# Optimization experiments

Measured on AMD Instinct MI355X. Metric: run time of the kernel, lower is better.

Reference implementation:

```python
import jax, jax.numpy as jnp
import numpy as np

B, L, D, H, E = 2, 2048, 1024, 4096, 8
CAP = int(1.25 * 2 * (B * L) / E)  # top-2 capacity = 1280


def setup_inputs() -> dict:
    key = jax.random.key(0)
    k0, k1, k2, k3 = jax.random.split(key, 4)
    gate_std = (0.1 / D) ** 0.5
    return {
        "inputs": jax.random.normal(k0, (B, L, D), jnp.float32),
        "gate_weight": jax.random.normal(k1, (E, D), jnp.float32) * gate_std,
        "w1": jax.random.normal(k2, (E, D, H), jnp.float32) * 0.02,
        "b1": jnp.zeros((E, 1, H), jnp.float32),
        "w2": jax.random.normal(k3, (E, H, D), jnp.float32) * 0.02,
        "b2": jnp.zeros((E, 1, D), jnp.float32),
    }


def reference(inputs, gate_weight, w1, b1, w2, b2):
    tokens = inputs.reshape(-1, D)                      # [S, D], S = B*L
    # gate computed in fp32 as in original
    logits = tokens.astype(jnp.float32) @ gate_weight.astype(jnp.float32).T  # [S, E]
    gates = jax.nn.softmax(logits, axis=-1)

    # top-2 routing
    top1 = jnp.argmax(gates, axis=-1)
    mask1 = jax.nn.one_hot(top1, E, dtype=jnp.float32)  # [S, E]
    gates_wo1 = jnp.where(mask1 > 0, -jnp.inf, gates)
    top2 = jnp.argmax(gates_wo1, axis=-1)
    mask2 = jax.nn.one_hot(top2, E, dtype=jnp.float32)

    # load-balancing aux loss (GShard style, pre-capacity masks)
    me = jnp.mean(gates, axis=0)
    ce = jnp.mean(mask1, axis=0)
    l_aux = E * jnp.sum(me * ce)

    # capacity positions via cumulative sum per expert
    loc1 = jnp.cumsum(mask1, axis=0) - 1.0              # [S, E]
    loc2 = jnp.cumsum(mask2, axis=0) - 1.0 + jnp.sum(mask1, axis=0, keepdims=True)
    mask1 = mask1 * (loc1 < CAP)
    mask2 = mask2 * (loc2 < CAP)

    gate1 = jnp.sum(gates * mask1, axis=-1)             # [S]
    gate2 = jnp.sum(gates * mask2, axis=-1)
    denom = jnp.maximum(gate1 + gate2, jnp.finfo(jnp.float32).eps)
    wgt1 = gate1 / denom
    wgt2 = gate2 / denom

    pos1 = jnp.sum(loc1 * mask1, axis=-1).astype(jnp.int32)  # [S]
    pos2 = jnp.sum(loc2 * mask2, axis=-1).astype(jnp.int32)
    cap1 = jax.nn.one_hot(pos1, CAP, dtype=jnp.float32)      # [S, C]
    cap2 = jax.nn.one_hot(pos2, CAP, dtype=jnp.float32)

    # combine weights [S, E, C] and dispatch mask
    combine = (wgt1[:, None, None] * mask1[:, :, None] * cap1[:, None, :]
               + wgt2[:, None, None] * mask2[:, :, None] * cap2[:, None, :])
    sec_mask_f = (combine > 0).astype(inputs.dtype)

    # dispatch: [E, C, S] @ [S, D] -> [E, C, D]
    dispatch = jnp.einsum('sec,sd->ecd', sec_mask_f, tokens)

    # per-expert FFN (batched over experts)
    h = jax.nn.gelu(jnp.einsum('ecd,edh->ech', dispatch, w1) + b1)
    expert_out = jnp.einsum('ech,ehd->ecd', h, w2) + b2

    # combine: [S, E*C] @ [E*C, D] -> [S, D]
    ans = jnp.einsum('sec,ecd->sd', combine.astype(inputs.dtype), expert_out)
    return ans.reshape(inputs.shape), l_aux
```

## Files before the change

### kernel.cpp

```cpp
#include <hip/hip_runtime.h>

#define S_TOK 4096
#define DMODEL 1024
#define HDIM 4096
#define NEXP 8
#define CAPACITY 1280

struct TokenRoute { int e1, p1, e2, p2; float w1, w2; };

typedef __bf16 bf16x8 __attribute__((ext_vector_type(8)));
typedef float f32x4 __attribute__((ext_vector_type(4)));
typedef unsigned short ushort8v __attribute__((ext_vector_type(8)));

__device__ __forceinline__ unsigned short f2bf(float f) {
    unsigned int u = __float_as_uint(f);
    unsigned int r = 0x7fffu + ((u >> 16) & 1u);
    return (unsigned short)((u + r) >> 16);
}
__device__ __forceinline__ float bf2f(unsigned short b) {
    return __uint_as_float(((unsigned int)b) << 16);
}

__device__ __forceinline__ void gload16(const void* gsrc, void* ldst) {
    __builtin_amdgcn_global_load_lds(
        (const __attribute__((address_space(1))) unsigned int*)gsrc,
        (__attribute__((address_space(3))) unsigned int*)ldst, 16, 0, 0);
}

template <int N> __device__ __forceinline__ void wait_vmcnt() {
    if constexpr (N == 0) asm volatile("s_waitcnt vmcnt(0)" ::: "memory");
    else if constexpr (N == 6) asm volatile("s_waitcnt vmcnt(6)" ::: "memory");
    else if constexpr (N == 8) asm volatile("s_waitcnt vmcnt(8)" ::: "memory");
}

__device__ __forceinline__ float gelu_f(float x) {
    float u = x * (0.7978845608028654f + 0.0356774081363f * x * x);
    return x / (1.0f + __expf(-2.0f * u));
}

__global__ void transpose_cvt(const float* __restrict__ src, unsigned short* __restrict__ dst,
                              int R, int C) {
    __shared__ unsigned short t[64][66];
    size_t eoff = (size_t)blockIdx.z * R * C;
    int r0 = blockIdx.y * 64, c0 = blockIdx.x * 64, tid = threadIdx.x;
    int rr = tid >> 4, cq = (tid & 15) * 4;
#pragma unroll
    for (int p = 0; p < 4; ++p) {
        int row = p * 16 + rr;
        float4 v = *(const float4*)(src + eoff + (size_t)(r0 + row) * C + c0 + cq);
        t[row][cq + 0] = f2bf(v.x); t[row][cq + 1] = f2bf(v.y);
        t[row][cq + 2] = f2bf(v.z); t[row][cq + 3] = f2bf(v.w);
    }
    __syncthreads();
    int k0 = (tid & 7) * 8;
#pragma unroll
    for (int pp = 0; pp < 2; ++pp) {
        int oc = pp * 32 + (tid >> 3);
        ushort8v o;
#pragma unroll
        for (int x = 0; x < 8; ++x) o[x] = t[k0 + x][oc];
        *(ushort8v*)(dst + eoff + (size_t)(c0 + oc) * R + r0 + k0) = o;
    }
}

__global__ void gate_kernel(const float* __restrict__ tokens, const float* __restrict__ gw,
                            float* __restrict__ gates, TokenRoute* __restrict__ route) {
    int s = blockIdx.x, l = threadIdx.x;
    const float* x = tokens + (size_t)s * DMODEL;
    float p[NEXP];
#pragma unroll
    for (int e = 0; e < NEXP; ++e) p[e] = 0.f;
#pragma unroll
    for (int it = 0; it < 4; ++it) {
        int i = (it * 64 + l) * 4;
        float4 v = *(const float4*)(x + i);
#pragma unroll
        for (int e = 0; e < NEXP; ++e) {
            float4 g = *(const float4*)(gw + e * DMODEL + i);
            p[e] += v.x * g.x + v.y * g.y + v.z * g.z + v.w * g.w;
        }
    }
#pragma unroll
    for (int e = 0; e < NEXP; ++e) {
        float v = p[e];
        v += __shfl_xor(v, 32); v += __shfl_xor(v, 16); v += __shfl_xor(v, 8);
        v += __shfl_xor(v, 4);  v += __shfl_xor(v, 2);  v += __shfl_xor(v, 1);
        p[e] = v;
    }
    int e1 = 0; float b1v = p[0];
#pragma unroll
    for (int e = 1; e < NEXP; ++e) if (p[e] > b1v) { b1v = p[e]; e1 = e; }
    int e2 = -1; float b2v = -3.0e38f;
#pragma unroll
    for (int e = 0; e < NEXP; ++e) if (e != e1 && p[e] > b2v) { b2v = p[e]; e2 = e; }
    float mx = p[0];
#pragma unroll
    for (int e = 1; e < NEXP; ++e) mx = fmaxf(mx, p[e]);
    float sum = 0.f;
#pragma unroll
    for (int e = 0; e < NEXP; ++e) { p[e] = __expf(p[e] - mx); sum += p[e]; }
    float inv = 1.0f / sum;
#pragma unroll
    for (int e = 0; e < NEXP; ++e) p[e] *= inv;
    float g1 = __expf(b1v - mx) * inv;
    float g2 = __expf(b2v - mx) * inv;
    if (l == 0) {
        float* gp = gates + (size_t)s * NEXP;
#pragma unroll
        for (int e = 0; e < NEXP; ++e) gp[e] = p[e];
        TokenRoute r; r.e1 = e1; r.p1 = 0; r.e2 = e2; r.p2 = 0; r.w1 = g1; r.w2 = g2;
        route[s] = r;
    }
}

__device__ __forceinline__ unsigned ext16(unsigned long long lo, unsigned long long hi, int e) {
    unsigned long long q = (e < 4) ? lo : hi;
    return (unsigned)((q >> ((e & 3) * 16)) & 0xFFFFULL);
}

__global__ __launch_bounds__(1024)
void route_scan(TokenRoute* __restrict__ route, const float* __restrict__ gates,
                int* __restrict__ cnt, float* __restrict__ laux_out) {
    __shared__ unsigned long long wt[16][4];
    __shared__ float fsum[16][NEXP];
    int t = threadIdx.x, wid = t >> 6, ln = t & 63;
    TokenRoute tr[4];
    unsigned long long own[4] = {0, 0, 0, 0};
#pragma unroll
    for (int j = 0; j < 4; ++j) {
        tr[j] = route[t * 4 + j];
        int e1 = tr[j].e1, e2 = tr[j].e2;
        if (e1 < 4) own[0] += 1ULL << (e1 * 16); else own[1] += 1ULL << ((e1 - 4) * 16);
        if (e2 < 4) own[2] += 1ULL << (e2 * 16); else own[3] += 1ULL << ((e2 - 4) * 16);
    }
    unsigned long long inc[4] = {own[0], own[1], own[2], own[3]};
#pragma unroll
    for (int off = 1; off < 64; off <<= 1) {
#pragma unroll
        for (int q = 0; q < 4; ++q) {
            unsigned long long v = __shfl_up(inc[q], off);
            if (ln >= off) inc[q] += v;
        }
    }
    if (ln == 63) {
#pragma unroll
        for (int q = 0; q < 4; ++q) wt[wid][q] = inc[q];
    }
    __syncthreads();
    unsigned long long woff[4] = {0, 0, 0, 0}, tot[4] = {0, 0, 0, 0};
    for (int w = 0; w < 16; ++w) {
#pragma unroll
        for (int q = 0; q < 4; ++q) {
            unsigned long long v = wt[w][q];
            tot[q] += v;
            if (w < wid) woff[q] += v;
        }
    }
    unsigned long long ex[4];
#pragma unroll
    for (int q = 0; q < 4; ++q) ex[q] = woff[q] + inc[q] - own[q];

    float gs[NEXP];
#pragma unroll
    for (int e = 0; e < NEXP; ++e) gs[e] = 0.f;
#pragma unroll
    for (int j = 0; j < 4; ++j) {
        const float* gp = gates + (size_t)(t * 4 + j) * NEXP;
#pragma unroll
        for (int e = 0; e < NEXP; ++e) gs[e] += gp[e];
    }
#pragma unroll
    for (int e = 0; e < NEXP; ++e) {
        float v = gs[e];
        v += __shfl_xor(v, 32); v += __shfl_xor(v, 16); v += __shfl_xor(v, 8);
        v += __shfl_xor(v, 4);  v += __shfl_xor(v, 2);  v += __shfl_xor(v, 1);
        gs[e] = v;
    }
    if (ln == 0) {
#pragma unroll
        for (int e = 0; e < NEXP; ++e) fsum[wid][e] = gs[e];
    }
    __syncthreads();
    if (t == 0) {
        float laux = 0.f;
#pragma unroll
        for (int e = 0; e < NEXP; ++e) {
            float m = 0.f;
            for (int w = 0; w < 16; ++w) m += fsum[w][e];
            unsigned t1 = ext16(tot[0], tot[1], e);
            unsigned t2 = ext16(tot[2], tot[3], e);
            laux += (m / (float)S_TOK) * ((float)t1 / (float)S_TOK);
            int c = (int)(t1 + t2);
            cnt[e] = c < CAPACITY ? c : CAPACITY;
        }
        *laux_out = laux * (float)NEXP;
    }
    unsigned long long r1lo = ex[0], r1hi = ex[1], r2lo = ex[2], r2hi = ex[3];
#pragma unroll
    for (int j = 0; j < 4; ++j) {
        int e1 = tr[j].e1, e2 = tr[j].e2;
        unsigned loc1 = ext16(r1lo, r1hi, e1);
        if (e1 < 4) r1lo += 1ULL << (e1 * 16); else r1hi += 1ULL << ((e1 - 4) * 16);
        unsigned loc2 = ext16(r2lo, r2hi, e2) + ext16(tot[0], tot[1], e2);
        if (e2 < 4) r2lo += 1ULL << (e2 * 16); else r2hi += 1ULL << ((e2 - 4) * 16);
        bool k1 = loc1 < CAPACITY, k2 = loc2 < CAPACITY;
        float G1 = k1 ? tr[j].w1 : 0.f;
        float G2 = k2 ? tr[j].w2 : 0.f;
        float denom = fmaxf(G1 + G2, 1.1920929e-07f);
        TokenRoute r;
        r.e1 = e1; r.p1 = k1 ? (int)loc1 : -1;
        r.e2 = e2; r.p2 = k2 ? (int)loc2 : -1;
        r.w1 = G1 / denom; r.w2 = G2 / denom;
        route[t * 4 + j] = r;
    }
}

__global__ void dispatch_scatter(const float* __restrict__ tokens, const TokenRoute* __restrict__ route,
                                 unsigned short* __restrict__ disp) {
    int s = blockIdx.x, l = threadIdx.x;
    TokenRoute r = route[s];
    const float* x = tokens + (size_t)s * DMODEL;
    ushort4 vals[4];
#pragma unroll
    for (int q = 0; q < 4; ++q) {
        float4 v = *(const float4*)(x + (q * 64 + l) * 4);
        vals[q].x = f2bf(v.x); vals[q].y = f2bf(v.y); vals[q].z = f2bf(v.z); vals[q].w = f2bf(v.w);
    }
    if (r.p1 >= 0) {
        unsigned short* d = disp + ((size_t)r.e1 * CAPACITY + r.p1) * DMODEL;
#pragma unroll
        for (int q = 0; q < 4; ++q) *(ushort4*)(d + (q * 64 + l) * 4) = vals[q];
    }
    if (r.p2 >= 0) {
        unsigned short* d = disp + ((size_t)r.e2 * CAPACITY + r.p2) * DMODEL;
#pragma unroll
        for (int q = 0; q < 4; ++q) *(ushort4*)(d + (q * 64 + l) * 4) = vals[q];
    }
}

template <int BN, int WM, int WN, int MODE>
__global__ __launch_bounds__(512, 2)
void gemm256(const unsigned short* __restrict__ A, const unsigned short* __restrict__ Bt,
             unsigned short* __restrict__ C, const float* __restrict__ bias,
             const int* __restrict__ cnt,
             int N, int K, int Ntiles,
             size_t strideAe, size_t strideBe, size_t strideCe, int biasStride) {
    constexpr int MF = 256 / WM / 16;
    constexpr int NF = BN / WN / 16;
    constexpr int RW = 256 / WM;
    constexpr int CW = BN / WN;
    constexpr int NBJ = BN / 64;
    constexpr int LPT = 4 + NBJ;
    constexpr int ASLOT = 256 * 64;
    constexpr int BSLOT = BN * 64;

    __shared__ unsigned short slds[(2 * 256 + 2 * BN) * 64];

    int e = blockIdx.z;
    int mt = blockIdx.x / Ntiles, nt = blockIdx.x % Ntiles;
    if (mt * 256 >= cnt[e]) return;
    const unsigned short* Ae = A + (size_t)e * strideAe;
    const unsigned short* Be = Bt + (size_t)e * strideBe;
    unsigned short* Ce = C + (size_t)e * strideCe;
    const float* be = bias + (size_t)e * biasStride;

    int tid = threadIdx.x;
    int wv = tid >> 6, ln = tid & 63;
    int wm = wv / WN, wn = wv % WN;
    int lr = ln & 15, kc = ln >> 4;
    int rsw = lr & 7;

    size_t gOffA[4]; int ldsA[4];
#pragma unroll
    for (int j = 0; j < 4; ++j) {
        int g = (wv * 4 + j) * 64 + ln;
        int row = g >> 3, cl = g & 7, cs = cl ^ (row & 7);
        ldsA[j] = (wv * 4 + j) * 512;
        gOffA[j] = (size_t)(mt * 256 + row) * K + cs * 8;
    }
    size_t gOffB[NBJ]; int ldsB[NBJ];
#pragma unroll
    for (int j = 0; j < NBJ; ++j) {
        int g = (wv * NBJ + j) * 64 + ln;
        int row = g >> 3, cl = g & 7, cs = cl ^ (row & 7);
        ldsB[j] = (wv * NBJ + j) * 512;
        gOffB[j] = (size_t)(nt * BN + row) * K + cs * 8;
    }
    int aoff[MF], boff[NF];
#pragma unroll
    for (int i = 0; i < MF; ++i) aoff[i] = (wm * RW + i * 16 + lr) * 64;
#pragma unroll
    for (int j = 0; j < NF; ++j) boff[j] = (wn * CW + j * 16 + lr) * 64;
    int chk0 = ((kc) ^ rsw) * 8;
    int chk1 = ((kc + 4) ^ rsw) * 8;

    f32x4 acc[MF][NF];
#pragma unroll
    for (int i = 0; i < MF; ++i)
#pragma unroll
        for (int j = 0; j < NF; ++j) acc[i][j] = (f32x4){0.f, 0.f, 0.f, 0.f};

    auto stage = [&](int slot, int kt) {
        unsigned short* da = slds + slot * ASLOT;
        unsigned short* db = slds + 2 * ASLOT + slot * BSLOT;
#pragma unroll
        for (int j = 0; j < 4; ++j) gload16(Ae + gOffA[j] + kt * 64, da + ldsA[j]);
#pragma unroll
        for (int j = 0; j < NBJ; ++j) gload16(Be + gOffB[j] + kt * 64, db + ldsB[j]);
    };

    int nk = K >> 6;
    stage(0, 0);
    stage(1, 1);
    wait_vmcnt<LPT>();
    __builtin_amdgcn_s_barrier();

    int cur = 0;
    for (int kt = 0; kt < nk; ++kt) {
        const unsigned short* sa = slds + cur * ASLOT;
        const unsigned short* sb = slds + 2 * ASLOT + cur * BSLOT;
        __builtin_amdgcn_s_setprio(1);
#pragma unroll
        for (int s = 0; s < 2; ++s) {
            int ck = (s == 0) ? chk0 : chk1;
            bf16x8 av[MF], bv[NF];
#pragma unroll
            for (int i = 0; i < MF; ++i) av[i] = *(const bf16x8*)(sa + aoff[i] + ck);
#pragma unroll
            for (int j = 0; j < NF; ++j) bv[j] = *(const bf16x8*)(sb + boff[j] + ck);
#pragma unroll
            for (int i = 0; i < MF; ++i)
#pragma unroll
                for (int j = 0; j < NF; ++j)
                    acc[i][j] = __builtin_amdgcn_mfma_f32_16x16x32_bf16(av[i], bv[j], acc[i][j], 0, 0, 0);
        }
        __builtin_amdgcn_s_setprio(0);
        __builtin_amdgcn_sched_barrier(0);
        __builtin_amdgcn_s_barrier();
        if (kt + 2 < nk) stage(cur, kt + 2);
        if (kt + 1 < nk) {
            if (kt + 2 < nk) wait_vmcnt<LPT>(); else wait_vmcnt<0>();
            __builtin_amdgcn_s_barrier();
        }
        cur ^= 1;
    }

    __syncthreads();
    unsigned short* scratch = slds + wv * (RW * CW);
    float bvj[NF];
#pragma unroll
    for (int j = 0; j < NF; ++j) bvj[j] = be[nt * BN + wn * CW + j * 16 + lr];
#pragma unroll
    for (int i = 0; i < MF; ++i) {
#pragma unroll
        for (int j = 0; j < NF; ++j) {
            int col_l = j * 16 + lr;
#pragma unroll
            for (int r = 0; r < 4; ++r) {
                int row_l = i * 16 + kc * 4 + r;
                float v = acc[i][j][r] + bvj[j];
                if (MODE == 0) v = gelu_f(v);
                scratch[row_l * CW + col_l] = f2bf(v);
            }
        }
    }
    int rrow = ln >> 3, rcol = (ln & 7) * 8;
#pragma unroll
    for (int p = 0; p < RW / 8; ++p) {
        int row_l = p * 8 + rrow;
        ushort8v v = *(const ushort8v*)&scratch[row_l * CW + rcol];
        int row_g = mt * 256 + wm * RW + row_l;
        int col_g = nt * BN + wn * CW + rcol;
        *(ushort8v*)&Ce[(size_t)row_g * N + col_g] = v;
    }
}

__global__ void combine_kernel(const TokenRoute* __restrict__ route, const unsigned short* __restrict__ eout,
                               float* __restrict__ out) {
    int s = blockIdx.x, l = threadIdx.x;
    TokenRoute r = route[s];
    bool v1 = r.p1 >= 0, v2 = r.p2 >= 0;
#pragma unroll
    for (int q = 0; q < 4; ++q) {
        int i = (q * 64 + l) * 4;
        float4 a = {0.f, 0.f, 0.f, 0.f};
        if (v1) {
            const unsigned short* p = eout + ((size_t)r.e1 * CAPACITY + r.p1) * DMODEL + i;
            ushort4 u = *(const ushort4*)p;
            a.x += r.w1 * bf2f(u.x); a.y += r.w1 * bf2f(u.y);
            a.z += r.w1 * bf2f(u.z); a.w += r.w1 * bf2f(u.w);
        }
        if (v2) {
            const unsigned short* p = eout + ((size_t)r.e2 * CAPACITY + r.p2) * DMODEL + i;
            ushort4 u = *(const ushort4*)p;
            a.x += r.w2 * bf2f(u.x); a.y += r.w2 * bf2f(u.y);
            a.z += r.w2 * bf2f(u.z); a.w += r.w2 * bf2f(u.w);
        }
        *(float4*)(out + (size_t)s * DMODEL + i) = a;
    }
}

extern "C" void kernel_launch(void* const* d_in, const int* in_sizes, int n_in,
                              void* d_out, int out_size, void* d_ws, size_t ws_size,
                              hipStream_t stream) {
    const float* inputs = (const float*)d_in[0];
    const float* gw     = (const float*)d_in[1];
    const float* w1     = (const float*)d_in[2];
    const float* b1     = (const float*)d_in[3];
    const float* w2     = (const float*)d_in[4];
    const float* b2     = (const float*)d_in[5];
    float* out = (float*)d_out;

    char* ws = (char*)d_ws;
    const size_t SZ_W = (size_t)NEXP * DMODEL * HDIM * 2;
    const size_t SZ_DISP = (size_t)NEXP * CAPACITY * DMODEL * 2;
    const size_t SZ_H = (size_t)NEXP * CAPACITY * HDIM * 2;
    unsigned short* wb1t = (unsigned short*)(ws);
    unsigned short* wb2t = (unsigned short*)(ws + SZ_W);
    unsigned short* disp = (unsigned short*)(ws + 2 * SZ_W);
    unsigned short* h    = (unsigned short*)(ws + 2 * SZ_W + SZ_DISP);
    float* gates = (float*)(ws + 2 * SZ_W + SZ_DISP + SZ_H);
    TokenRoute* route = (TokenRoute*)(ws + 2 * SZ_W + SZ_DISP + SZ_H + (size_t)S_TOK * NEXP * 4);
    int* cnt = (int*)((char*)route + (size_t)S_TOK * sizeof(TokenRoute));

    transpose_cvt<<<dim3(HDIM / 64, DMODEL / 64, NEXP), 256, 0, stream>>>(w1, wb1t, DMODEL, HDIM);
    transpose_cvt<<<dim3(DMODEL / 64, HDIM / 64, NEXP), 256, 0, stream>>>(w2, wb2t, HDIM, DMODEL);
    gate_kernel<<<S_TOK, 64, 0, stream>>>(inputs, gw, gates, route);
    route_scan<<<1, 1024, 0, stream>>>(route, gates, cnt, out + (size_t)S_TOK * DMODEL);
    dispatch_scatter<<<S_TOK, 64, 0, stream>>>(inputs, route, disp);
    gemm256<256, 2, 4, 0><<<dim3((CAPACITY / 256 + 1) * (HDIM / 256), 1, NEXP), 512, 0, stream>>>(
        disp, wb1t, h, b1, cnt, HDIM, DMODEL, HDIM / 256,
        (size_t)CAPACITY * DMODEL, (size_t)HDIM * DMODEL, (size_t)CAPACITY * HDIM, HDIM);
    gemm256<128, 4, 2, 1><<<dim3((CAPACITY / 256 + 1) * (DMODEL / 128), 1, NEXP), 512, 0, stream>>>(
        h, wb2t, disp, b2, cnt, DMODEL, HDIM, DMODEL / 128,
        (size_t)CAPACITY * HDIM, (size_t)DMODEL * HDIM, (size_t)CAPACITY * DMODEL, DMODEL);
    combine_kernel<<<S_TOK, 64, 0, stream>>>(route, disp, out);
}
```

Baseline: 642.5 us.

## Replace dispatch scatter with gathered GEMM, new triple-buffered 256x128 GEMM, fused gate+bf16 cvt

Removes the dispatch_scatter kernel. Tokens are converted to bf16 inside the gate kernel, and the first expert GEMM gathers rows through an index table built by a new idx_fill kernel. Both GEMMs move to a new 256-thread kernel with a 256x128 tile, K-step 32, a three-slot LDS pipeline, a row-pair swizzled layout and an XCD-aware block remap. The weight transpose kernel is rewritten for wider LDS accesses, and the expert output reuses the w1 workspace. Risks: gathered loads are less coalesced, and padded capacity rows index tokens through masked garbage indices.

After: 582.2 us. 9.4% less time.

```diff
diff --git a/kernel.cpp b/kernel.cpp
--- a/kernel.cpp
+++ b/kernel.cpp
@@ -30,7 +30,6 @@
 template <int N> __device__ __forceinline__ void wait_vmcnt() {
     if constexpr (N == 0) asm volatile("s_waitcnt vmcnt(0)" ::: "memory");
     else if constexpr (N == 6) asm volatile("s_waitcnt vmcnt(6)" ::: "memory");
-    else if constexpr (N == 8) asm volatile("s_waitcnt vmcnt(8)" ::: "memory");
 }
 
 __device__ __forceinline__ float gelu_f(float x) {
@@ -38,34 +37,41 @@
     return x / (1.0f + __expf(-2.0f * u));
 }
 
-__global__ void transpose_cvt(const float* __restrict__ src, unsigned short* __restrict__ dst,
-                              int R, int C) {
-    __shared__ unsigned short t[64][66];
+__global__ __launch_bounds__(256) void transpose_cvt(const float* __restrict__ src,
+                                                     unsigned short* __restrict__ dst,
+                                                     int R, int C) {
+    __shared__ unsigned short t2[64][72];
     size_t eoff = (size_t)blockIdx.z * R * C;
     int r0 = blockIdx.y * 64, c0 = blockIdx.x * 64, tid = threadIdx.x;
-    int rr = tid >> 4, cq = (tid & 15) * 4;
-#pragma unroll
-    for (int p = 0; p < 4; ++p) {
-        int row = p * 16 + rr;
-        float4 v = *(const float4*)(src + eoff + (size_t)(r0 + row) * C + c0 + cq);
-        t[row][cq + 0] = f2bf(v.x); t[row][cq + 1] = f2bf(v.y);
-        t[row][cq + 2] = f2bf(v.z); t[row][cq + 3] = f2bf(v.w);
+    int q = tid & 15, g = tid >> 4;
+    float vr[4][4];
+#pragma unroll
+    for (int rr = 0; rr < 4; ++rr) {
+        float4 v = *(const float4*)(src + eoff + (size_t)(r0 + g * 4 + rr) * C + c0 + q * 4);
+        vr[rr][0] = v.x; vr[rr][1] = v.y; vr[rr][2] = v.z; vr[rr][3] = v.w;
+    }
+#pragma unroll
+    for (int cc = 0; cc < 4; ++cc) {
+        ushort4 o;
+        o.x = f2bf(vr[0][cc]); o.y = f2bf(vr[1][cc]);
+        o.z = f2bf(vr[2][cc]); o.w = f2bf(vr[3][cc]);
+        *(ushort4*)&t2[q * 4 + cc][g * 4] = o;
     }
     __syncthreads();
-    int k0 = (tid & 7) * 8;
-#pragma unroll
-    for (int pp = 0; pp < 2; ++pp) {
-        int oc = pp * 32 + (tid >> 3);
-        ushort8v o;
-#pragma unroll
-        for (int x = 0; x < 8; ++x) o[x] = t[k0 + x][oc];
-        *(ushort8v*)(dst + eoff + (size_t)(c0 + oc) * R + r0 + k0) = o;
-    }
-}
-
-__global__ void gate_kernel(const float* __restrict__ tokens, const float* __restrict__ gw,
-                            float* __restrict__ gates, TokenRoute* __restrict__ route) {
-    int s = blockIdx.x, l = threadIdx.x;
+    int orr = tid >> 2, seg = tid & 3;
+    ushort8v a = *(const ushort8v*)&t2[orr][seg * 16];
+    ushort8v b = *(const ushort8v*)&t2[orr][seg * 16 + 8];
+    unsigned short* dp = dst + eoff + (size_t)(c0 + orr) * R + r0 + seg * 16;
+    *(ushort8v*)dp = a;
+    *(ushort8v*)(dp + 8) = b;
+}
+
+__global__ __launch_bounds__(256)
+void gate_cvt(const float* __restrict__ tokens, const float* __restrict__ gw,
+              unsigned short* __restrict__ tok, float* __restrict__ gates,
+              TokenRoute* __restrict__ route) {
+    int wv = threadIdx.x >> 6, l = threadIdx.x & 63;
+    int s = blockIdx.x * 4 + wv;
     const float* x = tokens + (size_t)s * DMODEL;
     float p[NEXP];
 #pragma unroll
@@ -74,10 +80,12 @@
     for (int it = 0; it < 4; ++it) {
         int i = (it * 64 + l) * 4;
         float4 v = *(const float4*)(x + i);
+        ushort4 o; o.x = f2bf(v.x); o.y = f2bf(v.y); o.z = f2bf(v.z); o.w = f2bf(v.w);
+        *(ushort4*)(tok + (size_t)s * DMODEL + i) = o;
 #pragma unroll
         for (int e = 0; e < NEXP; ++e) {
-            float4 g = *(const float4*)(gw + e * DMODEL + i);
-            p[e] += v.x * g.x + v.y * g.y + v.z * g.z + v.w * g.w;
+            float4 gg = *(const float4*)(gw + e * DMODEL + i);
+            p[e] += v.x * gg.x + v.y * gg.y + v.z * gg.z + v.w * gg.w;
         }
     }
 #pragma unroll
@@ -215,162 +223,141 @@
     }
 }
 
-__global__ void dispatch_scatter(const float* __restrict__ tokens, const TokenRoute* __restrict__ route,
-                                 unsigned short* __restrict__ disp) {
-    int s = blockIdx.x, l = threadIdx.x;
+__global__ void idx_fill(const TokenRoute* __restrict__ route, int* __restrict__ idx) {
+    int s = blockIdx.x * 256 + threadIdx.x;
     TokenRoute r = route[s];
-    const float* x = tokens + (size_t)s * DMODEL;
-    ushort4 vals[4];
-#pragma unroll
-    for (int q = 0; q < 4; ++q) {
-        float4 v = *(const float4*)(x + (q * 64 + l) * 4);
-        vals[q].x = f2bf(v.x); vals[q].y = f2bf(v.y); vals[q].z = f2bf(v.z); vals[q].w = f2bf(v.w);
-    }
-    if (r.p1 >= 0) {
-        unsigned short* d = disp + ((size_t)r.e1 * CAPACITY + r.p1) * DMODEL;
-#pragma unroll
-        for (int q = 0; q < 4; ++q) *(ushort4*)(d + (q * 64 + l) * 4) = vals[q];
-    }
-    if (r.p2 >= 0) {
-        unsigned short* d = disp + ((size_t)r.e2 * CAPACITY + r.p2) * DMODEL;
-#pragma unroll
-        for (int q = 0; q < 4; ++q) *(ushort4*)(d + (q * 64 + l) * 4) = vals[q];
-    }
-}
-
-template <int BN, int WM, int WN, int MODE>
-__global__ __launch_bounds__(512, 2)
-void gemm256(const unsigned short* __restrict__ A, const unsigned short* __restrict__ Bt,
-             unsigned short* __restrict__ C, const float* __restrict__ bias,
-             const int* __restrict__ cnt,
-             int N, int K, int Ntiles,
-             size_t strideAe, size_t strideBe, size_t strideCe, int biasStride) {
-    constexpr int MF = 256 / WM / 16;
-    constexpr int NF = BN / WN / 16;
-    constexpr int RW = 256 / WM;
-    constexpr int CW = BN / WN;
-    constexpr int NBJ = BN / 64;
-    constexpr int LPT = 4 + NBJ;
-    constexpr int ASLOT = 256 * 64;
-    constexpr int BSLOT = BN * 64;
-
-    __shared__ unsigned short slds[(2 * 256 + 2 * BN) * 64];
-
-    int e = blockIdx.z;
-    int mt = blockIdx.x / Ntiles, nt = blockIdx.x % Ntiles;
+    if (r.p1 >= 0) idx[r.e1 * CAPACITY + r.p1] = s;
+    if (r.p2 >= 0) idx[r.e2 * CAPACITY + r.p2] = s;
+}
+
+template <int KEL, int NT, bool GATHER, int MODE>
+__global__ __launch_bounds__(256, 2)
+void gemm_ff(const unsigned short* __restrict__ A, const int* __restrict__ idx,
+             const unsigned short* __restrict__ B, unsigned short* __restrict__ C,
+             const float* __restrict__ bias, const int* __restrict__ cnt,
+             int N, size_t strideAe, size_t strideBe, size_t strideCe, int biasStride) {
+    constexpr int NK = KEL / 32;
+    __shared__ unsigned short slds[3 * 8192 + 3 * 4096];
+
+    constexpr int TOTAL = NEXP * 5 * NT;
+    int bid = blockIdx.x;
+    int nb = (bid & 7) * (TOTAL >> 3) + (bid >> 3);
+    int nt = nb % NT; int mt = (nb / NT) % 5; int e = nb / (NT * 5);
     if (mt * 256 >= cnt[e]) return;
-    const unsigned short* Ae = A + (size_t)e * strideAe;
-    const unsigned short* Be = Bt + (size_t)e * strideBe;
+
+    const unsigned short* Ae = GATHER ? A : (A + (size_t)e * strideAe);
+    const unsigned short* Be = B + (size_t)e * strideBe + (size_t)nt * 128 * KEL;
     unsigned short* Ce = C + (size_t)e * strideCe;
     const float* be = bias + (size_t)e * biasStride;
 
-    int tid = threadIdx.x;
-    int wv = tid >> 6, ln = tid & 63;
-    int wm = wv / WN, wn = wv % WN;
-    int lr = ln & 15, kc = ln >> 4;
-    int rsw = lr & 7;
-
-    size_t gOffA[4]; int ldsA[4];
+    int tid = threadIdx.x, wv = tid >> 6, ln = tid & 63;
+    int wm = wv >> 1, wn = wv & 1;
+    int lr = ln & 15, kc4 = ln >> 4;
+
+    const unsigned short* gAp[4]; int ldsA[4];
+#pragma unroll
+    for (int jj = 0; jj < 4; ++jj) {
+        int p = (wv * 4 + jj) * 64 + ln;
+        int lq = p >> 3, c = p & 7, u = c ^ (lq & 7);
+        int r = 2 * lq + (u >> 2), kcs = u & 3;
+        ldsA[jj] = p * 8;
+        if constexpr (GATHER) {
+            int tokr = idx[e * CAPACITY + mt * 256 + r] & (S_TOK - 1);
+            gAp[jj] = Ae + (size_t)tokr * KEL + kcs * 8;
+        } else {
+            gAp[jj] = Ae + (size_t)(mt * 256 + r) * KEL + kcs * 8;
+        }
+    }
+    const unsigned short* gBp[2]; int ldsB[2];
+#pragma unroll
+    for (int jj = 0; jj < 2; ++jj) {
+        int p = (wv * 2 + jj) * 64 + ln;
+        int lq = p >> 3, c = p & 7, u = c ^ (lq & 7);
+        int r = 2 * lq + (u >> 2), kcs = u & 3;
+        ldsB[jj] = p * 8;
+        gBp[jj] = Be + (size_t)r * KEL + kcs * 8;
+    }
+    int aoff[8], boff[4];
+#pragma unroll
+    for (int i = 0; i < 8; ++i) {
+        int row = wm * 128 + i * 16 + lr;
+        int lq = row >> 1, c = (((lr & 1) << 2) | kc4) ^ (lq & 7);
+        aoff[i] = lq * 64 + c * 8;
+    }
 #pragma unroll
     for (int j = 0; j < 4; ++j) {
-        int g = (wv * 4 + j) * 64 + ln;
-        int row = g >> 3, cl = g & 7, cs = cl ^ (row & 7);
-        ldsA[j] = (wv * 4 + j) * 512;
-        gOffA[j] = (size_t)(mt * 256 + row) * K + cs * 8;
-    }
-    size_t gOffB[NBJ]; int ldsB[NBJ];
-#pragma unroll
-    for (int j = 0; j < NBJ; ++j) {
-        int g = (wv * NBJ + j) * 64 + ln;
-        int row = g >> 3, cl = g & 7, cs = cl ^ (row & 7);
-        ldsB[j] = (wv * NBJ + j) * 512;
-        gOffB[j] = (size_t)(nt * BN + row) * K + cs * 8;
-    }
-    int aoff[MF], boff[NF];
-#pragma unroll
-    for (int i = 0; i < MF; ++i) aoff[i] = (wm * RW + i * 16 + lr) * 64;
-#pragma unroll
-    for (int j = 0; j < NF; ++j) boff[j] = (wn * CW + j * 16 + lr) * 64;
-    int chk0 = ((kc) ^ rsw) * 8;
-    int chk1 = ((kc + 4) ^ rsw) * 8;
-
-    f32x4 acc[MF][NF];
-#pragma unroll
-    for (int i = 0; i < MF; ++i)
-#pragma unroll
-        for (int j = 0; j < NF; ++j) acc[i][j] = (f32x4){0.f, 0.f, 0.f, 0.f};
-
-    auto stage = [&](int slot, int kt) {
-        unsigned short* da = slds + slot * ASLOT;
-        unsigned short* db = slds + 2 * ASLOT + slot * BSLOT;
-#pragma unroll
-        for (int j = 0; j < 4; ++j) gload16(Ae + gOffA[j] + kt * 64, da + ldsA[j]);
-#pragma unroll
-        for (int j = 0; j < NBJ; ++j) gload16(Be + gOffB[j] + kt * 64, db + ldsB[j]);
+        int row = wn * 64 + j * 16 + lr;
+        int lq = row >> 1, c = (((lr & 1) << 2) | kc4) ^ (lq & 7);
+        boff[j] = lq * 64 + c * 8;
+    }
+
+    f32x4 acc[8][4];
+#pragma unroll
+    for (int i = 0; i < 8; ++i)
+#pragma unroll
+        for (int j = 0; j < 4; ++j) acc[i][j] = (f32x4){0.f, 0.f, 0.f, 0.f};
+
+    auto stage = [&](int kt, int slot) {
+#pragma unroll
+        for (int jj = 0; jj < 4; ++jj)
+            gload16(gAp[jj] + kt * 32, &slds[slot * 8192 + ldsA[jj]]);
+#pragma unroll
+        for (int jj = 0; jj < 2; ++jj)
+            gload16(gBp[jj] + kt * 32, &slds[24576 + slot * 4096 + ldsB[jj]]);
     };
 
-    int nk = K >> 6;
     stage(0, 0);
     stage(1, 1);
-    wait_vmcnt<LPT>();
+    wait_vmcnt<6>();
     __builtin_amdgcn_s_barrier();
 
-    int cur = 0;
-    for (int kt = 0; kt < nk; ++kt) {
-        const unsigned short* sa = slds + cur * ASLOT;
-        const unsigned short* sb = slds + 2 * ASLOT + cur * BSLOT;
+    int sc = 0;
+    for (int kt = 0; kt < NK; ++kt) {
+        int s2 = sc + 2; if (s2 >= 3) s2 -= 3;
+        if (kt + 2 < NK) stage(kt + 2, s2);
+        bf16x8 av[8], bv[4];
+#pragma unroll
+        for (int i = 0; i < 8; ++i) av[i] = *(const bf16x8*)&slds[sc * 8192 + aoff[i]];
+#pragma unroll
+        for (int j = 0; j < 4; ++j) bv[j] = *(const bf16x8*)&slds[24576 + sc * 4096 + boff[j]];
         __builtin_amdgcn_s_setprio(1);
 #pragma unroll
-        for (int s = 0; s < 2; ++s) {
-            int ck = (s == 0) ? chk0 : chk1;
-            bf16x8 av[MF], bv[NF];
-#pragma unroll
-            for (int i = 0; i < MF; ++i) av[i] = *(const bf16x8*)(sa + aoff[i] + ck);
-#pragma unroll
-            for (int j = 0; j < NF; ++j) bv[j] = *(const bf16x8*)(sb + boff[j] + ck);
-#pragma unroll
-            for (int i = 0; i < MF; ++i)
-#pragma unroll
-                for (int j = 0; j < NF; ++j)
-                    acc[i][j] = __builtin_amdgcn_mfma_f32_16x16x32_bf16(av[i], bv[j], acc[i][j], 0, 0, 0);
-        }
+        for (int i = 0; i < 8; ++i)
+#pragma unroll
+            for (int j = 0; j < 4; ++j)
+                acc[i][j] = __builtin_amdgcn_mfma_f32_16x16x32_bf16(av[i], bv[j], acc[i][j], 0, 0, 0);
         __builtin_amdgcn_s_setprio(0);
-        __builtin_amdgcn_sched_barrier(0);
+        if (kt + 2 < NK) wait_vmcnt<6>();
+        else wait_vmcnt<0>();
         __builtin_amdgcn_s_barrier();
-        if (kt + 2 < nk) stage(cur, kt + 2);
-        if (kt + 1 < nk) {
-            if (kt + 2 < nk) wait_vmcnt<LPT>(); else wait_vmcnt<0>();
-            __builtin_amdgcn_s_barrier();
-        }
-        cur ^= 1;
+        sc = (sc == 2) ? 0 : sc + 1;
     }
 
     __syncthreads();
-    unsigned short* scratch = slds + wv * (RW * CW);
-    float bvj[NF];
-#pragma unroll
-    for (int j = 0; j < NF; ++j) bvj[j] = be[nt * BN + wn * CW + j * 16 + lr];
-#pragma unroll
-    for (int i = 0; i < MF; ++i) {
-#pragma unroll
-        for (int j = 0; j < NF; ++j) {
-            int col_l = j * 16 + lr;
+    unsigned short* scratch = slds + wv * 8192;
+    float bvj[4];
+#pragma unroll
+    for (int j = 0; j < 4; ++j) bvj[j] = be[nt * 128 + wn * 64 + j * 16 + lr];
+#pragma unroll
+    for (int i = 0; i < 8; ++i) {
+#pragma unroll
+        for (int j = 0; j < 4; ++j) {
 #pragma unroll
             for (int r = 0; r < 4; ++r) {
-                int row_l = i * 16 + kc * 4 + r;
-                float v = acc[i][j][r] + bvj[j];
-                if (MODE == 0) v = gelu_f(v);
-                scratch[row_l * CW + col_l] = f2bf(v);
+                float vv = acc[i][j][r] + bvj[j];
+                if (MODE == 0) vv = gelu_f(vv);
+                scratch[(i * 16 + kc4 * 4 + r) * 64 + j * 16 + lr] = f2bf(vv);
             }
         }
     }
+    __syncthreads();
     int rrow = ln >> 3, rcol = (ln & 7) * 8;
 #pragma unroll
-    for (int p = 0; p < RW / 8; ++p) {
+    for (int p = 0; p < 16; ++p) {
         int row_l = p * 8 + rrow;
-        ushort8v v = *(const ushort8v*)&scratch[row_l * CW + rcol];
-        int row_g = mt * 256 + wm * RW + row_l;
-        int col_g = nt * BN + wn * CW + rcol;
+        ushort8v v = *(const ushort8v*)&scratch[row_l * 64 + rcol];
+        int row_g = mt * 256 + wm * 128 + row_l;
+        int col_g = nt * 128 + wn * 64 + rcol;
         *(ushort8v*)&Ce[(size_t)row_g * N + col_g] = v;
     }
 }
@@ -412,27 +399,29 @@
     float* out = (float*)d_out;
 
     char* ws = (char*)d_ws;
-    const size_t SZ_W = (size_t)NEXP * DMODEL * HDIM * 2;
-    const size_t SZ_DISP = (size_t)NEXP * CAPACITY * DMODEL * 2;
-    const size_t SZ_H = (size_t)NEXP * CAPACITY * HDIM * 2;
+    const size_t SZ_W   = (size_t)NEXP * DMODEL * HDIM * 2;
+    const size_t SZ_H   = (size_t)NEXP * CAPACITY * HDIM * 2;
+    const size_t SZ_TOK = (size_t)S_TOK * DMODEL * 2;
     unsigned short* wb1t = (unsigned short*)(ws);
     unsigned short* wb2t = (unsigned short*)(ws + SZ_W);
-    unsigned short* disp = (unsigned short*)(ws + 2 * SZ_W);
-    unsigned short* h    = (unsigned short*)(ws + 2 * SZ_W + SZ_DISP);
-    float* gates = (float*)(ws + 2 * SZ_W + SZ_DISP + SZ_H);
-    TokenRoute* route = (TokenRoute*)(ws + 2 * SZ_W + SZ_DISP + SZ_H + (size_t)S_TOK * NEXP * 4);
+    unsigned short* h    = (unsigned short*)(ws + 2 * SZ_W);
+    unsigned short* tok  = (unsigned short*)(ws + 2 * SZ_W + SZ_H);
+    float* gates = (float*)(ws + 2 * SZ_W + SZ_H + SZ_TOK);
+    TokenRoute* route = (TokenRoute*)((char*)gates + (size_t)S_TOK * NEXP * 4);
     int* cnt = (int*)((char*)route + (size_t)S_TOK * sizeof(TokenRoute));
+    int* idxb = (int*)((char*)cnt + 128);
+    unsigned short* eout = wb1t;
 
     transpose_cvt<<<dim3(HDIM / 64, DMODEL / 64, NEXP), 256, 0, stream>>>(w1, wb1t, DMODEL, HDIM);
     transpose_cvt<<<dim3(DMODEL / 64, HDIM / 64, NEXP), 256, 0, stream>>>(w2, wb2t, HDIM, DMODEL);
-    gate_kernel<<<S_TOK, 64, 0, stream>>>(inputs, gw, gates, route);
+    gate_cvt<<<S_TOK / 4, 256, 0, stream>>>(inputs, gw, tok, gates, route);
     route_scan<<<1, 1024, 0, stream>>>(route, gates, cnt, out + (size_t)S_TOK * DMODEL);
-    dispatch_scatter<<<S_TOK, 64, 0, stream>>>(inputs, route, disp);
-    gemm256<256, 2, 4, 0><<<dim3((CAPACITY / 256 + 1) * (HDIM / 256), 1, NEXP), 512, 0, stream>>>(
-        disp, wb1t, h, b1, cnt, HDIM, DMODEL, HDIM / 256,
-        (size_t)CAPACITY * DMODEL, (size_t)HDIM * DMODEL, (size_t)CAPACITY * HDIM, HDIM);
-    gemm256<128, 4, 2, 1><<<dim3((CAPACITY / 256 + 1) * (DMODEL / 128), 1, NEXP), 512, 0, stream>>>(
-        h, wb2t, disp, b2, cnt, DMODEL, HDIM, DMODEL / 128,
+    idx_fill<<<S_TOK / 256, 256, 0, stream>>>(route, idxb);
+    gemm_ff<DMODEL, 32, true, 0><<<NEXP * 5 * 32, 256, 0, stream>>>(
+        tok, idxb, wb1t, h, b1, cnt, HDIM,
+        0, (size_t)HDIM * DMODEL, (size_t)CAPACITY * HDIM, HDIM);
+    gemm_ff<HDIM, 8, false, 1><<<NEXP * 5 * 8, 256, 0, stream>>>(
+        h, idxb, wb2t, eout, b2, cnt, DMODEL,
         (size_t)CAPACITY * HDIM, (size_t)DMODEL * HDIM, (size_t)CAPACITY * DMODEL, DMODEL);
-    combine_kernel<<<S_TOK, 64, 0, stream>>>(route, disp, out);
-}
+    combine_kernel<<<S_TOK, 64, 0, stream>>>(route, eout, out);
+}
```
